# Optimization experiments

Hardware: AMD Instinct MI355X
Metric: run time of the kernel (lower is better)

Reference implementation:

```python
import jax, jax.numpy as jnp
import numpy as np

D_MODEL = 512
D_K = 64
D_V = 64
N_HEADS = 8
N = 4096
EPS = 1e-5


def setup_inputs() -> dict:
    key = jax.random.key(0)
    ks = jax.random.split(key, 12)
    s = 1.0 / np.sqrt(D_MODEL)
    return {
        "Q": jax.random.normal(ks[0], (N, D_MODEL), dtype=jnp.float32),
        "K": jax.random.normal(ks[1], (N, D_MODEL), dtype=jnp.float32),
        "V": jax.random.normal(ks[2], (N, D_MODEL), dtype=jnp.float32),
        "W_Q": jax.random.normal(ks[3], (D_K * N_HEADS, D_MODEL), dtype=jnp.float32) * s,
        "b_Q": jnp.zeros((D_K * N_HEADS,), jnp.float32),
        "W_K": jax.random.normal(ks[4], (D_K * N_HEADS, D_MODEL), dtype=jnp.float32) * s,
        "b_K": jnp.zeros((D_K * N_HEADS,), jnp.float32),
        "W_V": jax.random.normal(ks[5], (D_V * N_HEADS, D_MODEL), dtype=jnp.float32) * s,
        "b_V": jnp.zeros((D_V * N_HEADS,), jnp.float32),
        "W_O": jax.random.normal(ks[6], (D_MODEL, N_HEADS * D_V), dtype=jnp.float32) * s,
        "b_O": jnp.zeros((D_MODEL,), jnp.float32),
        "gamma": jnp.ones((D_MODEL,), jnp.float32),
        "beta": jnp.zeros((D_MODEL,), jnp.float32),
    }


def reference(Q, K, V, W_Q, b_Q, W_K, b_K, W_V, b_V, W_O, b_O, gamma, beta):
    n = Q.shape[0]
    # projections (torch Linear: x @ W.T + b), then split heads: [N, H, dk]
    Qs = (Q @ W_Q.T + b_Q).reshape(n, N_HEADS, D_K)
    Ks = (K @ W_K.T + b_K).reshape(n, N_HEADS, D_K)
    Vs = (V @ W_V.T + b_V).reshape(n, N_HEADS, D_V)
    # per-head scaled dot-product attention over the N dim, batched via einsum
    scores = jnp.einsum("nhd,mhd->hnm", Qs, Ks) / np.sqrt(D_K)  # [H, N, N]
    attn = jax.nn.softmax(scores, axis=-1)
    ctx = jnp.einsum("hnm,mhd->nhd", attn, Vs)  # [N, H, dv]
    context = ctx.reshape(n, N_HEADS * D_V)  # concat heads (matches torch.cat order)
    out = context @ W_O.T + b_O + Q  # output proj + residual
    # LayerNorm over last dim
    mu = jnp.mean(out, axis=-1, keepdims=True)
    var = jnp.mean((out - mu) ** 2, axis=-1, keepdims=True)
    return (out - mu) * jax.lax.rsqrt(var + EPS) * gamma + beta
```

## Files before the change

### kernel.cpp

```cpp
#include <hip/hip_runtime.h>
#include <cstdint>

#define N_TOK 4096
#define DMODEL 512
#define NHEADS 8
#define HDIM 64

typedef unsigned short u16;
typedef __bf16 bf16x8 __attribute__((ext_vector_type(8)));
typedef float f32x4 __attribute__((ext_vector_type(4)));

union U128 { uint4 u; bf16x8 b; u16 s[8]; };

__device__ __forceinline__ u16 f2bf(float f) {
  uint32_t u = __builtin_bit_cast(uint32_t, f);
  u += 0x7FFFu + ((u >> 16) & 1u);
  return (u16)(u >> 16);
}
__device__ __forceinline__ u16 bfr(float f) {
  uint32_t u = __builtin_bit_cast(uint32_t, f);
  return (u16)((u + 0x8000u) >> 16);
}
__device__ __forceinline__ float bf2f(u16 s) {
  uint32_t u = ((uint32_t)s) << 16;
  return __builtin_bit_cast(float, u);
}

#if __has_builtin(__builtin_amdgcn_exp2f)
#define EXP2(x) __builtin_amdgcn_exp2f(x)
#else
#define EXP2(x) __expf((x) * 0.6931471805599453f)
#endif

__device__ __forceinline__ void ldg2lds16(const void* g, void* s) {
  __builtin_amdgcn_global_load_lds(
      (const __attribute__((address_space(1))) void*)g,
      (__attribute__((address_space(3))) void*)s, 16, 0, 0);
}

__global__ __launch_bounds__(256) void cvt3_kernel(
    const float* __restrict__ a0, const float* __restrict__ a1, const float* __restrict__ a2,
    u16* __restrict__ b0, u16* __restrict__ b1, u16* __restrict__ b2)
{
  const float* src = (blockIdx.y == 0) ? a0 : (blockIdx.y == 1) ? a1 : a2;
  u16* dst         = (blockIdx.y == 0) ? b0 : (blockIdx.y == 1) ? b1 : b2;
  int i = (blockIdx.x * 256 + threadIdx.x) * 4;
  float4 f = *(const float4*)(src + i);
  ushort4 o;
  o.x = f2bf(f.x); o.y = f2bf(f.y); o.z = f2bf(f.z); o.w = f2bf(f.w);
  *(ushort4*)(dst + i) = o;
}

__global__ __launch_bounds__(256) void proj3_kernel(
    const u16* __restrict__ Qb, const u16* __restrict__ Kb, const u16* __restrict__ Vb,
    const float* __restrict__ WQ, const float* __restrict__ WK, const float* __restrict__ WV,
    const float* __restrict__ bQ, const float* __restrict__ bK, const float* __restrict__ bV,
    u16* __restrict__ Qs, u16* __restrict__ Ks, u16* __restrict__ Vt)
{
  const int z = blockIdx.z;
  const u16* A      = (z == 0) ? Qb : (z == 1) ? Kb : Vb;
  const float* W    = (z == 0) ? WQ : (z == 1) ? WK : WV;
  const float* bias = (z == 0) ? bQ : (z == 1) ? bK : bV;

  const int m0 = blockIdx.x * 128;
  const int j0 = blockIdx.y * 64;
  const int tid = threadIdx.x;
  const int w = tid >> 6, lane = tid & 63, quad = lane >> 4, l = lane & 15;

  __shared__ bf16x8 sA[8][128];
  __shared__ bf16x8 sB[8][64];

  const f32x4 zero = {0.f, 0.f, 0.f, 0.f};
  f32x4 acc[2][4];
#pragma unroll
  for (int m = 0; m < 2; ++m)
#pragma unroll
    for (int s = 0; s < 4; ++s) acc[m][s] = zero;

  const int brow0 = tid >> 3;
  const int bc    = tid & 7;

  for (int k0 = 0; k0 < DMODEL; k0 += 64) {
    __syncthreads();
#pragma unroll
    for (int i = 0; i < 4; ++i) {
      const int chunk = 2 * w + (i >> 1), half = (i & 1) * 64;
      const u16* ag = A + (size_t)(m0 + half + lane) * DMODEL + k0 + chunk * 8;
      ldg2lds16(ag, (char*)sA + (size_t)(chunk * 128 + half) * 16);
    }
#pragma unroll
    for (int i = 0; i < 2; ++i) {
      const int row = brow0 + 32 * i;
      const float* wp = W + (size_t)(j0 + row) * DMODEL + k0 + bc * 8;
      float4 g0 = *(const float4*)wp;
      float4 g1 = *(const float4*)(wp + 4);
      U128 v;
      v.s[0]=f2bf(g0.x); v.s[1]=f2bf(g0.y); v.s[2]=f2bf(g0.z); v.s[3]=f2bf(g0.w);
      v.s[4]=f2bf(g1.x); v.s[5]=f2bf(g1.y); v.s[6]=f2bf(g1.z); v.s[7]=f2bf(g1.w);
      sB[bc][row] = v.b;
    }
    __syncthreads();
#pragma unroll
    for (int c = 0; c < 2; ++c) {
      bf16x8 af0 = sA[c * 4 + quad][w * 32 + l];
      bf16x8 af1 = sA[c * 4 + quad][w * 32 + 16 + l];
#pragma unroll
      for (int s = 0; s < 4; ++s) {
        bf16x8 bfb = sB[c * 4 + quad][s * 16 + l];
        acc[0][s] = __builtin_amdgcn_mfma_f32_16x16x32_bf16(af0, bfb, acc[0][s], 0, 0, 0);
        acc[1][s] = __builtin_amdgcn_mfma_f32_16x16x32_bf16(af1, bfb, acc[1][s], 0, 0, 0);
      }
    }
  }

#pragma unroll
  for (int m = 0; m < 2; ++m)
#pragma unroll
    for (int s = 0; s < 4; ++s) {
      int j = j0 + s * 16 + l;
      float bv = bias[j];
      int n0 = m0 + w * 32 + m * 16 + quad * 4;
      if (z < 2) {
        u16* Y = (z == 0) ? Qs : Ks;
#pragma unroll
        for (int r = 0; r < 4; ++r)
          Y[(size_t)(n0 + r) * DMODEL + j] = f2bf(acc[m][s][r] + bv);
      } else {
        ushort4 pk;
        pk.x = f2bf(acc[m][s][0] + bv); pk.y = f2bf(acc[m][s][1] + bv);
        pk.z = f2bf(acc[m][s][2] + bv); pk.w = f2bf(acc[m][s][3] + bv);
        *(ushort4*)(Vt + (size_t)j * N_TOK + n0) = pk;
      }
    }
}

__global__ __launch_bounds__(512, 4) void attn_kernel(
    const u16* __restrict__ Qs, const u16* __restrict__ Ks,
    const u16* __restrict__ Vt, float* __restrict__ Opart, float* __restrict__ Lpart)
{
  const int qt = blockIdx.x, h = blockIdx.y, split = blockIdx.z;
  const int tid = threadIdx.x;
  const int w = tid >> 6, lane = tid & 63, quad = lane >> 4, l = lane & 15;

  __shared__ bf16x8 kch[8][64];
  __shared__ bf16x8 vch[8][64];
  __shared__ __align__(16) u16 pbuf[8][32][72];

  const int wq0 = qt * 256 + w * 32;

  bf16x8 qf[2][2];
#pragma unroll
  for (int c = 0; c < 2; ++c)
#pragma unroll
    for (int m = 0; m < 2; ++m) {
      U128 u;
      u.u = *(const uint4*)(Qs + (size_t)(wq0 + m * 16 + l) * DMODEL + h * HDIM + c * 32 + quad * 8);
#pragma unroll
      for (int j = 0; j < 8; ++j) u.s[j] = f2bf(bf2f(u.s[j]) * 0.18033688f);
      qf[c][m] = u.b;
    }

  const f32x4 zero = {0.f, 0.f, 0.f, 0.f};
  f32x4 o[2][4];
  float lsum[2] = {0.f, 0.f};
#pragma unroll
  for (int m = 0; m < 2; ++m)
#pragma unroll
    for (int s = 0; s < 4; ++s) o[m][s] = zero;

  for (int it = 0; it < 16; ++it) {
    const int j0 = split * 1024 + it * 64;
    __syncthreads();
    if (w < 4) {
      const u16* kg = Ks + (size_t)(j0 + lane) * DMODEL + h * HDIM + w * 16;
      ldg2lds16(kg,     (char*)kch + w * 2048);
      ldg2lds16(kg + 8, (char*)kch + w * 2048 + 1024);
    } else {
      const int w2 = w - 4;
      const u16* vg = Vt + (size_t)(h * HDIM + lane) * N_TOK + j0 + w2 * 16;
      ldg2lds16(vg,     (char*)vch + w2 * 2048);
      ldg2lds16(vg + 8, (char*)vch + w2 * 2048 + 1024);
    }
    __syncthreads();

    f32x4 sacc[2][4];
#pragma unroll
    for (int m = 0; m < 2; ++m)
#pragma unroll
      for (int t = 0; t < 4; ++t) sacc[m][t] = zero;
#pragma unroll
    for (int c = 0; c < 2; ++c) {
#pragma unroll
      for (int t = 0; t < 4; ++t) {
        bf16x8 kf = kch[c * 4 + quad][t * 16 + l];
        sacc[0][t] = __builtin_amdgcn_mfma_f32_16x16x32_bf16(kf, qf[c][0], sacc[0][t], 0, 0, 0);
        sacc[1][t] = __builtin_amdgcn_mfma_f32_16x16x32_bf16(kf, qf[c][1], sacc[1][t], 0, 0, 0);
      }
    }

#pragma unroll
    for (int m = 0; m < 2; ++m) {
#pragma unroll
      for (int t = 0; t < 4; ++t) {
        float p0 = EXP2(sacc[m][t][0]);
        float p1 = EXP2(sacc[m][t][1]);
        float p2 = EXP2(sacc[m][t][2]);
        float p3 = EXP2(sacc[m][t][3]);
        lsum[m] += (p0 + p1) + (p2 + p3);
        ushort4 pk;
        pk.x = bfr(p0); pk.y = bfr(p1); pk.z = bfr(p2); pk.w = bfr(p3);
        *(ushort4*)&pbuf[w][m * 16 + l][t * 16 + quad * 4] = pk;
      }
    }

#pragma unroll
    for (int c = 0; c < 2; ++c) {
      U128 u0, u1;
      u0.u = *(const uint4*)&pbuf[w][l][c * 32 + quad * 8];
      u1.u = *(const uint4*)&pbuf[w][16 + l][c * 32 + quad * 8];
#pragma unroll
      for (int s = 0; s < 4; ++s) {
        bf16x8 vf = vch[c * 4 + quad][s * 16 + l];
        o[0][s] = __builtin_amdgcn_mfma_f32_16x16x32_bf16(u0.b, vf, o[0][s], 0, 0, 0);
        o[1][s] = __builtin_amdgcn_mfma_f32_16x16x32_bf16(u1.b, vf, o[1][s], 0, 0, 0);
      }
    }
  }

#pragma unroll
  for (int m = 0; m < 2; ++m) {
    lsum[m] += __shfl_xor(lsum[m], 16);
    lsum[m] += __shfl_xor(lsum[m], 32);
  }
  if (quad == 0) {
    Lpart[((size_t)split * NHEADS + h) * N_TOK + wq0 + l]      = lsum[0];
    Lpart[((size_t)split * NHEADS + h) * N_TOK + wq0 + 16 + l] = lsum[1];
  }
  float* Ob = Opart + (size_t)((split * NHEADS + h) * 16 + qt) * 16384;
#pragma unroll
  for (int m = 0; m < 2; ++m)
#pragma unroll
    for (int s = 0; s < 4; ++s)
#pragma unroll
      for (int r = 0; r < 4; ++r)
        Ob[(w * 32 + m * 16 + quad * 4 + r) * 64 + s * 16 + l] = o[m][s][r];
}

__global__ __launch_bounds__(256) void combine_kernel(
    const float* __restrict__ Opart, const float* __restrict__ Lpart,
    u16* __restrict__ ctx)
{
  int idx = blockIdx.x * 256 + threadIdx.x;
  int n = idx >> 6;
  int c8 = idx & 63;
  int h = c8 >> 3;
  int vd0 = (c8 & 7) * 8;
  int qt = n >> 8, qin = n & 255;

  float acc[8] = {0, 0, 0, 0, 0, 0, 0, 0};
  float lsum = 0.f;
#pragma unroll
  for (int s = 0; s < 4; ++s) {
    size_t base = (size_t)((s * NHEADS + h) * 16 + qt) * 16384 + qin * 64 + vd0;
    float4 a = *(const float4*)(Opart + base);
    float4 b = *(const float4*)(Opart + base + 4);
    acc[0] += a.x; acc[1] += a.y; acc[2] += a.z; acc[3] += a.w;
    acc[4] += b.x; acc[5] += b.y; acc[6] += b.z; acc[7] += b.w;
    lsum += Lpart[((size_t)s * NHEADS + h) * N_TOK + n];
  }
  float inv = 1.f / lsum;
  U128 u;
#pragma unroll
  for (int j = 0; j < 8; ++j) u.s[j] = f2bf(acc[j] * inv);
  *(uint4*)(ctx + (size_t)n * DMODEL + h * HDIM + vd0) = u.u;
}

__global__ __launch_bounds__(256) void gemmo_kernel(
    const u16* __restrict__ ctx, const float* __restrict__ WO,
    const float* __restrict__ bO, const float* __restrict__ resid,
    float* __restrict__ Y)
{
  const int m0 = blockIdx.x * 64;
  const int j0 = blockIdx.y * 64;
  const int tid = threadIdx.x;
  const int w = tid >> 6, lane = tid & 63, quad = lane >> 4, l = lane & 15;

  __shared__ bf16x8 sA[8][64];
  __shared__ bf16x8 sB[8][64];

  const f32x4 zero = {0.f, 0.f, 0.f, 0.f};
  f32x4 acc[4];
  for (int s = 0; s < 4; ++s) acc[s] = zero;

  const int brow0 = tid >> 3;
  const int bc    = tid & 7;

  for (int k0 = 0; k0 < DMODEL; k0 += 64) {
    __syncthreads();
#pragma unroll
    for (int i = 0; i < 2; ++i) {
      const u16* ag = ctx + (size_t)(m0 + lane) * DMODEL + k0 + (2 * w + i) * 8;
      ldg2lds16(ag, (char*)sA + (size_t)(2 * w + i) * 1024);
    }
#pragma unroll
    for (int i = 0; i < 2; ++i) {
      const int row = brow0 + 32 * i;
      const float* wp = WO + (size_t)(j0 + row) * DMODEL + k0 + bc * 8;
      float4 g0 = *(const float4*)wp;
      float4 g1 = *(const float4*)(wp + 4);
      U128 v;
      v.s[0]=f2bf(g0.x); v.s[1]=f2bf(g0.y); v.s[2]=f2bf(g0.z); v.s[3]=f2bf(g0.w);
      v.s[4]=f2bf(g1.x); v.s[5]=f2bf(g1.y); v.s[6]=f2bf(g1.z); v.s[7]=f2bf(g1.w);
      sB[bc][row] = v.b;
    }
    __syncthreads();
#pragma unroll
    for (int c = 0; c < 2; ++c) {
      bf16x8 af = sA[c * 4 + quad][w * 16 + l];
#pragma unroll
      for (int s = 0; s < 4; ++s) {
        bf16x8 bfb = sB[c * 4 + quad][s * 16 + l];
        acc[s] = __builtin_amdgcn_mfma_f32_16x16x32_bf16(af, bfb, acc[s], 0, 0, 0);
      }
    }
  }
#pragma unroll
  for (int s = 0; s < 4; ++s) {
    int j = j0 + s * 16 + l;
    float bv = bO[j];
#pragma unroll
    for (int r = 0; r < 4; ++r) {
      int n = m0 + w * 16 + quad * 4 + r;
      Y[(size_t)n * DMODEL + j] = acc[s][r] + bv + resid[(size_t)n * DMODEL + j];
    }
  }
}

__global__ __launch_bounds__(256) void ln_kernel(
    const float* __restrict__ X, const float* __restrict__ gamma,
    const float* __restrict__ beta, float* __restrict__ Y)
{
  const int w = threadIdx.x >> 6, lane = threadIdx.x & 63;
  const int row = blockIdx.x * 4 + w;
  const float* x = X + (size_t)row * DMODEL + lane * 8;
  float4 a = *(const float4*)x;
  float4 b = *(const float4*)(x + 4);

  float s = a.x + a.y + a.z + a.w + b.x + b.y + b.z + b.w;
#pragma unroll
  for (int m = 1; m < 64; m <<= 1) s += __shfl_xor(s, m);
  float mu = s * (1.f / DMODEL);

  float d0 = a.x - mu, d1 = a.y - mu, d2 = a.z - mu, d3 = a.w - mu;
  float d4 = b.x - mu, d5 = b.y - mu, d6 = b.z - mu, d7 = b.w - mu;
  float v = d0*d0 + d1*d1 + d2*d2 + d3*d3 + d4*d4 + d5*d5 + d6*d6 + d7*d7;
#pragma unroll
  for (int m = 1; m < 64; m <<= 1) v += __shfl_xor(v, m);
  float sc = rsqrtf(v * (1.f / DMODEL) + 1e-5f);

  const float* g = gamma + lane * 8;
  const float* be = beta + lane * 8;
  float4 go = *(const float4*)g;
  float4 g1 = *(const float4*)(g + 4);
  float4 bo = *(const float4*)be;
  float4 b1 = *(const float4*)(be + 4);

  float4 y0, y1;
  y0.x = d0 * sc * go.x + bo.x;  y0.y = d1 * sc * go.y + bo.y;
  y0.z = d2 * sc * go.z + bo.z;  y0.w = d3 * sc * go.w + bo.w;
  y1.x = d4 * sc * g1.x + b1.x;  y1.y = d5 * sc * g1.y + b1.y;
  y1.z = d6 * sc * g1.z + b1.z;  y1.w = d7 * sc * g1.w + b1.w;

  float* yp = Y + (size_t)row * DMODEL + lane * 8;
  *(float4*)yp = y0;
  *(float4*)(yp + 4) = y1;
}

extern "C" void kernel_launch(void* const* d_in, const int* in_sizes, int n_in,
                              void* d_out, int out_size, void* d_ws, size_t ws_size,
                              hipStream_t stream)
{
  const float* Q     = (const float*)d_in[0];
  const float* K     = (const float*)d_in[1];
  const float* V     = (const float*)d_in[2];
  const float* WQ    = (const float*)d_in[3];
  const float* bQ    = (const float*)d_in[4];
  const float* WK    = (const float*)d_in[5];
  const float* bK    = (const float*)d_in[6];
  const float* WV    = (const float*)d_in[7];
  const float* bV    = (const float*)d_in[8];
  const float* WO    = (const float*)d_in[9];
  const float* bO    = (const float*)d_in[10];
  const float* gamma = (const float*)d_in[11];
  const float* beta  = (const float*)d_in[12];

  const size_t MB = 1ull << 20;
  char* ws = (char*)d_ws;
  u16* Qb   = (u16*)(ws + 0 * MB);
  u16* Kb   = (u16*)(ws + 4 * MB);
  u16* Vb   = (u16*)(ws + 8 * MB);
  u16* Qs   = (u16*)(ws + 12 * MB);
  u16* Ks   = (u16*)(ws + 16 * MB);
  u16* Vt   = (u16*)(ws + 20 * MB);
  u16* ctx  = (u16*)(ws + 24 * MB);
  float* Opart = (float*)(ws + 28 * MB);
  float* tmp   = (float*)(ws + 28 * MB);
  float* Lpart = (float*)(ws + 60 * MB);
  float* out = (float*)d_out;

  cvt3_kernel<<<dim3(2048, 3), 256, 0, stream>>>(Q, K, V, Qb, Kb, Vb);
  proj3_kernel<<<dim3(32, 8, 3), 256, 0, stream>>>(Qb, Kb, Vb, WQ, WK, WV,
                                                   bQ, bK, bV, Qs, Ks, Vt);
  attn_kernel<<<dim3(16, 8, 4), 512, 0, stream>>>(Qs, Ks, Vt, Opart, Lpart);
  combine_kernel<<<1024, 256, 0, stream>>>(Opart, Lpart, ctx);
  gemmo_kernel<<<dim3(64, 8), 256, 0, stream>>>(ctx, WO, bO, Q, tmp);
  ln_kernel<<<1024, 256, 0, stream>>>(tmp, gamma, beta, out);
}
```

Measured before the change: 187.5 us.

## Fuse input conversion into projection, widen attention tiles, store bf16 partials

Removes the separate fp32-to-bf16 conversion kernel and converts Q/K/V inside the projection GEMM while loading them into a padded LDS tile. The attention kernel moves to 256 threads with 64 query rows per wave, interleaves score and exp per key subtile, truncates P to bf16, and writes split partial outputs as bf16 in a contiguous layout. The combine kernel reads these bf16 partials, and the output GEMM uses 128-row tiles. This cuts launches and memory traffic at the cost of more register pressure in attention and lower precision in the partials.

```diff
diff --git a/kernel.cpp b/kernel.cpp
--- a/kernel.cpp
+++ b/kernel.cpp
@@ -17,14 +17,12 @@
   u += 0x7FFFu + ((u >> 16) & 1u);
   return (u16)(u >> 16);
 }
-__device__ __forceinline__ u16 bfr(float f) {
-  uint32_t u = __builtin_bit_cast(uint32_t, f);
-  return (u16)((u + 0x8000u) >> 16);
-}
 __device__ __forceinline__ float bf2f(u16 s) {
   uint32_t u = ((uint32_t)s) << 16;
   return __builtin_bit_cast(float, u);
 }
+__device__ __forceinline__ float bitf(uint32_t u) { return __builtin_bit_cast(float, u); }
+__device__ __forceinline__ uint32_t fbit(float f) { return __builtin_bit_cast(uint32_t, f); }
 
 #if __has_builtin(__builtin_amdgcn_exp2f)
 #define EXP2(x) __builtin_amdgcn_exp2f(x)
@@ -38,27 +36,14 @@
       (__attribute__((address_space(3))) void*)s, 16, 0, 0);
 }
 
-__global__ __launch_bounds__(256) void cvt3_kernel(
-    const float* __restrict__ a0, const float* __restrict__ a1, const float* __restrict__ a2,
-    u16* __restrict__ b0, u16* __restrict__ b1, u16* __restrict__ b2)
-{
-  const float* src = (blockIdx.y == 0) ? a0 : (blockIdx.y == 1) ? a1 : a2;
-  u16* dst         = (blockIdx.y == 0) ? b0 : (blockIdx.y == 1) ? b1 : b2;
-  int i = (blockIdx.x * 256 + threadIdx.x) * 4;
-  float4 f = *(const float4*)(src + i);
-  ushort4 o;
-  o.x = f2bf(f.x); o.y = f2bf(f.y); o.z = f2bf(f.z); o.w = f2bf(f.w);
-  *(ushort4*)(dst + i) = o;
-}
-
 __global__ __launch_bounds__(256) void proj3_kernel(
-    const u16* __restrict__ Qb, const u16* __restrict__ Kb, const u16* __restrict__ Vb,
+    const float* __restrict__ Qin, const float* __restrict__ Kin, const float* __restrict__ Vin,
     const float* __restrict__ WQ, const float* __restrict__ WK, const float* __restrict__ WV,
     const float* __restrict__ bQ, const float* __restrict__ bK, const float* __restrict__ bV,
     u16* __restrict__ Qs, u16* __restrict__ Ks, u16* __restrict__ Vt)
 {
   const int z = blockIdx.z;
-  const u16* A      = (z == 0) ? Qb : (z == 1) ? Kb : Vb;
+  const float* A    = (z == 0) ? Qin : (z == 1) ? Kin : Vin;
   const float* W    = (z == 0) ? WQ : (z == 1) ? WK : WV;
   const float* bias = (z == 0) ? bQ : (z == 1) ? bK : bV;
 
@@ -67,7 +52,7 @@
   const int tid = threadIdx.x;
   const int w = tid >> 6, lane = tid & 63, quad = lane >> 4, l = lane & 15;
 
-  __shared__ bf16x8 sA[8][128];
+  __shared__ __align__(16) u16 sAu[8 * 129 * 8];
   __shared__ bf16x8 sB[8][64];
 
   const f32x4 zero = {0.f, 0.f, 0.f, 0.f};
@@ -83,10 +68,16 @@
   for (int k0 = 0; k0 < DMODEL; k0 += 64) {
     __syncthreads();
 #pragma unroll
-    for (int i = 0; i < 4; ++i) {
-      const int chunk = 2 * w + (i >> 1), half = (i & 1) * 64;
-      const u16* ag = A + (size_t)(m0 + half + lane) * DMODEL + k0 + chunk * 8;
-      ldg2lds16(ag, (char*)sA + (size_t)(chunk * 128 + half) * 16);
+    for (int i = 0; i < 8; ++i) {
+      int flat4 = i * 256 + tid;
+      int f = flat4 * 4;
+      int row = f >> 6;
+      int col = f & 63;
+      float4 fv = *(const float4*)(A + (size_t)(m0 + row) * DMODEL + k0 + col);
+      ushort4 hh;
+      hh.x = f2bf(fv.x); hh.y = f2bf(fv.y); hh.z = f2bf(fv.z); hh.w = f2bf(fv.w);
+      int chunk = col >> 3, half = (col >> 2) & 1;
+      *(ushort4*)(sAu + ((chunk * 129 + row) << 3) + half * 4) = hh;
     }
 #pragma unroll
     for (int i = 0; i < 2; ++i) {
@@ -102,8 +93,8 @@
     __syncthreads();
 #pragma unroll
     for (int c = 0; c < 2; ++c) {
-      bf16x8 af0 = sA[c * 4 + quad][w * 32 + l];
-      bf16x8 af1 = sA[c * 4 + quad][w * 32 + 16 + l];
+      bf16x8 af0 = *(const bf16x8*)(sAu + (((c * 4 + quad) * 129 + w * 32 + l) << 3));
+      bf16x8 af1 = *(const bf16x8*)(sAu + (((c * 4 + quad) * 129 + w * 32 + 16 + l) << 3));
 #pragma unroll
       for (int s = 0; s < 4; ++s) {
         bf16x8 bfb = sB[c * 4 + quad][s * 16 + l];
@@ -134,9 +125,9 @@
     }
 }
 
-__global__ __launch_bounds__(512, 4) void attn_kernel(
+__global__ __launch_bounds__(256, 2) void attn_kernel(
     const u16* __restrict__ Qs, const u16* __restrict__ Ks,
-    const u16* __restrict__ Vt, float* __restrict__ Opart, float* __restrict__ Lpart)
+    const u16* __restrict__ Vt, u16* __restrict__ Opart, float* __restrict__ Lpart)
 {
   const int qt = blockIdx.x, h = blockIdx.y, split = blockIdx.z;
   const int tid = threadIdx.x;
@@ -144,15 +135,15 @@
 
   __shared__ bf16x8 kch[8][64];
   __shared__ bf16x8 vch[8][64];
-  __shared__ __align__(16) u16 pbuf[8][32][72];
-
-  const int wq0 = qt * 256 + w * 32;
-
-  bf16x8 qf[2][2];
+  __shared__ __align__(16) u16 pbuf[4][64][88];
+
+  const int wq0 = qt * 256 + w * 64;
+
+  bf16x8 qf[2][4];
 #pragma unroll
   for (int c = 0; c < 2; ++c)
 #pragma unroll
-    for (int m = 0; m < 2; ++m) {
+    for (int m = 0; m < 4; ++m) {
       U128 u;
       u.u = *(const uint4*)(Qs + (size_t)(wq0 + m * 16 + l) * DMODEL + h * HDIM + c * 32 + quad * 8);
 #pragma unroll
@@ -161,93 +152,100 @@
     }
 
   const f32x4 zero = {0.f, 0.f, 0.f, 0.f};
-  f32x4 o[2][4];
-  float lsum[2] = {0.f, 0.f};
-#pragma unroll
-  for (int m = 0; m < 2; ++m)
+  f32x4 o[4][4];
+  float lsum[4] = {0.f, 0.f, 0.f, 0.f};
+#pragma unroll
+  for (int m = 0; m < 4; ++m)
 #pragma unroll
     for (int s = 0; s < 4; ++s) o[m][s] = zero;
 
   for (int it = 0; it < 16; ++it) {
     const int j0 = split * 1024 + it * 64;
     __syncthreads();
-    if (w < 4) {
-      const u16* kg = Ks + (size_t)(j0 + lane) * DMODEL + h * HDIM + w * 16;
-      ldg2lds16(kg,     (char*)kch + w * 2048);
-      ldg2lds16(kg + 8, (char*)kch + w * 2048 + 1024);
+    if (w < 2) {
+#pragma unroll
+      for (int i = 0; i < 4; ++i) {
+        const int chunk = w * 4 + i;
+        const u16* kg = Ks + (size_t)(j0 + lane) * DMODEL + h * HDIM + chunk * 8;
+        ldg2lds16(kg, (char*)kch + chunk * 1024);
+      }
     } else {
-      const int w2 = w - 4;
-      const u16* vg = Vt + (size_t)(h * HDIM + lane) * N_TOK + j0 + w2 * 16;
-      ldg2lds16(vg,     (char*)vch + w2 * 2048);
-      ldg2lds16(vg + 8, (char*)vch + w2 * 2048 + 1024);
-    }
-    __syncthreads();
-
-    f32x4 sacc[2][4];
-#pragma unroll
-    for (int m = 0; m < 2; ++m)
-#pragma unroll
-      for (int t = 0; t < 4; ++t) sacc[m][t] = zero;
+#pragma unroll
+      for (int i = 0; i < 4; ++i) {
+        const int chunk = (w - 2) * 4 + i;
+        const u16* vg = Vt + (size_t)(h * HDIM + lane) * N_TOK + j0 + chunk * 8;
+        ldg2lds16(vg, (char*)vch + chunk * 1024);
+      }
+    }
+    __syncthreads();
+
+#pragma unroll
+    for (int t = 0; t < 4; ++t) {
+      f32x4 sacc[4];
+#pragma unroll
+      for (int m = 0; m < 4; ++m) sacc[m] = zero;
+#pragma unroll
+      for (int c = 0; c < 2; ++c) {
+        bf16x8 kf = kch[c * 4 + quad][t * 16 + l];
+        sacc[0] = __builtin_amdgcn_mfma_f32_16x16x32_bf16(kf, qf[c][0], sacc[0], 0, 0, 0);
+        sacc[1] = __builtin_amdgcn_mfma_f32_16x16x32_bf16(kf, qf[c][1], sacc[1], 0, 0, 0);
+        sacc[2] = __builtin_amdgcn_mfma_f32_16x16x32_bf16(kf, qf[c][2], sacc[2], 0, 0, 0);
+        sacc[3] = __builtin_amdgcn_mfma_f32_16x16x32_bf16(kf, qf[c][3], sacc[3], 0, 0, 0);
+      }
+#pragma unroll
+      for (int m = 0; m < 4; ++m) {
+        uint32_t u0 = fbit(EXP2(sacc[m][0]));
+        uint32_t u1 = fbit(EXP2(sacc[m][1]));
+        uint32_t u2 = fbit(EXP2(sacc[m][2]));
+        uint32_t u3 = fbit(EXP2(sacc[m][3]));
+        uint32_t pk01 = (u0 >> 16) | (u1 & 0xFFFF0000u);
+        uint32_t pk23 = (u2 >> 16) | (u3 & 0xFFFF0000u);
+        lsum[m] += (bitf(pk01 << 16) + bitf(pk01 & 0xFFFF0000u)) +
+                   (bitf(pk23 << 16) + bitf(pk23 & 0xFFFF0000u));
+        uint2 st; st.x = pk01; st.y = pk23;
+        *(uint2*)&pbuf[w][m * 16 + l][t * 16 + quad * 4] = st;
+      }
+    }
+
 #pragma unroll
     for (int c = 0; c < 2; ++c) {
-#pragma unroll
-      for (int t = 0; t < 4; ++t) {
-        bf16x8 kf = kch[c * 4 + quad][t * 16 + l];
-        sacc[0][t] = __builtin_amdgcn_mfma_f32_16x16x32_bf16(kf, qf[c][0], sacc[0][t], 0, 0, 0);
-        sacc[1][t] = __builtin_amdgcn_mfma_f32_16x16x32_bf16(kf, qf[c][1], sacc[1][t], 0, 0, 0);
-      }
-    }
-
-#pragma unroll
-    for (int m = 0; m < 2; ++m) {
-#pragma unroll
-      for (int t = 0; t < 4; ++t) {
-        float p0 = EXP2(sacc[m][t][0]);
-        float p1 = EXP2(sacc[m][t][1]);
-        float p2 = EXP2(sacc[m][t][2]);
-        float p3 = EXP2(sacc[m][t][3]);
-        lsum[m] += (p0 + p1) + (p2 + p3);
-        ushort4 pk;
-        pk.x = bfr(p0); pk.y = bfr(p1); pk.z = bfr(p2); pk.w = bfr(p3);
-        *(ushort4*)&pbuf[w][m * 16 + l][t * 16 + quad * 4] = pk;
-      }
-    }
-
-#pragma unroll
-    for (int c = 0; c < 2; ++c) {
-      U128 u0, u1;
-      u0.u = *(const uint4*)&pbuf[w][l][c * 32 + quad * 8];
-      u1.u = *(const uint4*)&pbuf[w][16 + l][c * 32 + quad * 8];
+      U128 pf[4];
+#pragma unroll
+      for (int m = 0; m < 4; ++m)
+        pf[m].u = *(const uint4*)&pbuf[w][m * 16 + l][c * 32 + quad * 8];
 #pragma unroll
       for (int s = 0; s < 4; ++s) {
         bf16x8 vf = vch[c * 4 + quad][s * 16 + l];
-        o[0][s] = __builtin_amdgcn_mfma_f32_16x16x32_bf16(u0.b, vf, o[0][s], 0, 0, 0);
-        o[1][s] = __builtin_amdgcn_mfma_f32_16x16x32_bf16(u1.b, vf, o[1][s], 0, 0, 0);
-      }
-    }
-  }
-
-#pragma unroll
-  for (int m = 0; m < 2; ++m) {
+        o[0][s] = __builtin_amdgcn_mfma_f32_16x16x32_bf16(pf[0].b, vf, o[0][s], 0, 0, 0);
+        o[1][s] = __builtin_amdgcn_mfma_f32_16x16x32_bf16(pf[1].b, vf, o[1][s], 0, 0, 0);
+        o[2][s] = __builtin_amdgcn_mfma_f32_16x16x32_bf16(pf[2].b, vf, o[2][s], 0, 0, 0);
+        o[3][s] = __builtin_amdgcn_mfma_f32_16x16x32_bf16(pf[3].b, vf, o[3][s], 0, 0, 0);
+      }
+    }
+  }
+
+#pragma unroll
+  for (int m = 0; m < 4; ++m) {
     lsum[m] += __shfl_xor(lsum[m], 16);
     lsum[m] += __shfl_xor(lsum[m], 32);
   }
   if (quad == 0) {
-    Lpart[((size_t)split * NHEADS + h) * N_TOK + wq0 + l]      = lsum[0];
-    Lpart[((size_t)split * NHEADS + h) * N_TOK + wq0 + 16 + l] = lsum[1];
-  }
-  float* Ob = Opart + (size_t)((split * NHEADS + h) * 16 + qt) * 16384;
-#pragma unroll
-  for (int m = 0; m < 2; ++m)
+#pragma unroll
+    for (int m = 0; m < 4; ++m)
+      Lpart[((size_t)split * NHEADS + h) * N_TOK + wq0 + m * 16 + l] = lsum[m];
+  }
+  u16* Ob = Opart + ((size_t)(split * NHEADS + h) * N_TOK + wq0) * 64;
+#pragma unroll
+  for (int m = 0; m < 4; ++m)
 #pragma unroll
     for (int s = 0; s < 4; ++s)
 #pragma unroll
       for (int r = 0; r < 4; ++r)
-        Ob[(w * 32 + m * 16 + quad * 4 + r) * 64 + s * 16 + l] = o[m][s][r];
+        Ob[(size_t)(m * 16 + quad * 4 + r) * 64 + s * 16 + l] = f2bf(o[m][s][r]);
 }
 
 __global__ __launch_bounds__(256) void combine_kernel(
-    const float* __restrict__ Opart, const float* __restrict__ Lpart,
+    const u16* __restrict__ Opart, const float* __restrict__ Lpart,
     u16* __restrict__ ctx)
 {
   int idx = blockIdx.x * 256 + threadIdx.x;
@@ -255,17 +253,15 @@
   int c8 = idx & 63;
   int h = c8 >> 3;
   int vd0 = (c8 & 7) * 8;
-  int qt = n >> 8, qin = n & 255;
 
   float acc[8] = {0, 0, 0, 0, 0, 0, 0, 0};
   float lsum = 0.f;
 #pragma unroll
   for (int s = 0; s < 4; ++s) {
-    size_t base = (size_t)((s * NHEADS + h) * 16 + qt) * 16384 + qin * 64 + vd0;
-    float4 a = *(const float4*)(Opart + base);
-    float4 b = *(const float4*)(Opart + base + 4);
-    acc[0] += a.x; acc[1] += a.y; acc[2] += a.z; acc[3] += a.w;
-    acc[4] += b.x; acc[5] += b.y; acc[6] += b.z; acc[7] += b.w;
+    U128 u;
+    u.u = *(const uint4*)(Opart + ((size_t)(s * NHEADS + h) * N_TOK + n) * 64 + vd0);
+#pragma unroll
+    for (int j = 0; j < 8; ++j) acc[j] += bf2f(u.s[j]);
     lsum += Lpart[((size_t)s * NHEADS + h) * N_TOK + n];
   }
   float inv = 1.f / lsum;
@@ -280,17 +276,20 @@
     const float* __restrict__ bO, const float* __restrict__ resid,
     float* __restrict__ Y)
 {
-  const int m0 = blockIdx.x * 64;
+  const int m0 = blockIdx.x * 128;
   const int j0 = blockIdx.y * 64;
   const int tid = threadIdx.x;
   const int w = tid >> 6, lane = tid & 63, quad = lane >> 4, l = lane & 15;
 
-  __shared__ bf16x8 sA[8][64];
+  __shared__ bf16x8 sA[8][128];
   __shared__ bf16x8 sB[8][64];
 
   const f32x4 zero = {0.f, 0.f, 0.f, 0.f};
-  f32x4 acc[4];
-  for (int s = 0; s < 4; ++s) acc[s] = zero;
+  f32x4 acc[2][4];
+#pragma unroll
+  for (int m = 0; m < 2; ++m)
+#pragma unroll
+    for (int s = 0; s < 4; ++s) acc[m][s] = zero;
 
   const int brow0 = tid >> 3;
   const int bc    = tid & 7;
@@ -298,9 +297,10 @@
   for (int k0 = 0; k0 < DMODEL; k0 += 64) {
     __syncthreads();
 #pragma unroll
-    for (int i = 0; i < 2; ++i) {
-      const u16* ag = ctx + (size_t)(m0 + lane) * DMODEL + k0 + (2 * w + i) * 8;
-      ldg2lds16(ag, (char*)sA + (size_t)(2 * w + i) * 1024);
+    for (int i = 0; i < 4; ++i) {
+      const int chunk = 2 * w + (i >> 1), half = (i & 1) * 64;
+      const u16* ag = ctx + (size_t)(m0 + half + lane) * DMODEL + k0 + chunk * 8;
+      ldg2lds16(ag, (char*)sA + (size_t)(chunk * 128 + half) * 16);
     }
 #pragma unroll
     for (int i = 0; i < 2; ++i) {
@@ -316,24 +316,27 @@
     __syncthreads();
 #pragma unroll
     for (int c = 0; c < 2; ++c) {
-      bf16x8 af = sA[c * 4 + quad][w * 16 + l];
+      bf16x8 af0 = sA[c * 4 + quad][w * 32 + l];
+      bf16x8 af1 = sA[c * 4 + quad][w * 32 + 16 + l];
 #pragma unroll
       for (int s = 0; s < 4; ++s) {
         bf16x8 bfb = sB[c * 4 + quad][s * 16 + l];
-        acc[s] = __builtin_amdgcn_mfma_f32_16x16x32_bf16(af, bfb, acc[s], 0, 0, 0);
-      }
-    }
-  }
-#pragma unroll
-  for (int s = 0; s < 4; ++s) {
-    int j = j0 + s * 16 + l;
-    float bv = bO[j];
-#pragma unroll
-    for (int r = 0; r < 4; ++r) {
-      int n = m0 + w * 16 + quad * 4 + r;
-      Y[(size_t)n * DMODEL + j] = acc[s][r] + bv + resid[(size_t)n * DMODEL + j];
-    }
-  }
+        acc[0][s] = __builtin_amdgcn_mfma_f32_16x16x32_bf16(af0, bfb, acc[0][s], 0, 0, 0);
+        acc[1][s] = __builtin_amdgcn_mfma_f32_16x16x32_bf16(af1, bfb, acc[1][s], 0, 0, 0);
+      }
+    }
+  }
+#pragma unroll
+  for (int m = 0; m < 2; ++m)
+#pragma unroll
+    for (int s = 0; s < 4; ++s) {
+      int j = j0 + s * 16 + l;
+      float bv = bO[j];
+      int n0 = m0 + w * 32 + m * 16 + quad * 4;
+#pragma unroll
+      for (int r = 0; r < 4; ++r)
+        Y[(size_t)(n0 + r) * DMODEL + j] = acc[m][s][r] + bv + resid[(size_t)(n0 + r) * DMODEL + j];
+    }
 }
 
 __global__ __launch_bounds__(256) void ln_kernel(
@@ -396,23 +399,19 @@
 
   const size_t MB = 1ull << 20;
   char* ws = (char*)d_ws;
-  u16* Qb   = (u16*)(ws + 0 * MB);
-  u16* Kb   = (u16*)(ws + 4 * MB);
-  u16* Vb   = (u16*)(ws + 8 * MB);
-  u16* Qs   = (u16*)(ws + 12 * MB);
-  u16* Ks   = (u16*)(ws + 16 * MB);
-  u16* Vt   = (u16*)(ws + 20 * MB);
-  u16* ctx  = (u16*)(ws + 24 * MB);
-  float* Opart = (float*)(ws + 28 * MB);
-  float* tmp   = (float*)(ws + 28 * MB);
-  float* Lpart = (float*)(ws + 60 * MB);
+  u16* Qs   = (u16*)(ws + 0 * MB);
+  u16* Ks   = (u16*)(ws + 4 * MB);
+  u16* Vt   = (u16*)(ws + 8 * MB);
+  u16* ctx  = (u16*)(ws + 12 * MB);
+  u16* Opart = (u16*)(ws + 16 * MB);
+  float* tmp = (float*)(ws + 16 * MB);
+  float* Lpart = (float*)(ws + 32 * MB);
   float* out = (float*)d_out;
 
-  cvt3_kernel<<<dim3(2048, 3), 256, 0, stream>>>(Q, K, V, Qb, Kb, Vb);
-  proj3_kernel<<<dim3(32, 8, 3), 256, 0, stream>>>(Qb, Kb, Vb, WQ, WK, WV,
+  proj3_kernel<<<dim3(32, 8, 3), 256, 0, stream>>>(Q, K, V, WQ, WK, WV,
                                                    bQ, bK, bV, Qs, Ks, Vt);
-  attn_kernel<<<dim3(16, 8, 4), 512, 0, stream>>>(Qs, Ks, Vt, Opart, Lpart);
+  attn_kernel<<<dim3(16, 8, 4), 256, 0, stream>>>(Qs, Ks, Vt, Opart, Lpart);
   combine_kernel<<<1024, 256, 0, stream>>>(Opart, Lpart, ctx);
-  gemmo_kernel<<<dim3(64, 8), 256, 0, stream>>>(ctx, WO, bO, Q, tmp);
+  gemmo_kernel<<<dim3(32, 8), 256, 0, stream>>>(ctx, WO, bO, Q, tmp);
   ln_kernel<<<1024, 256, 0, stream>>>(tmp, gamma, beta, out);
 }
```

Result: slower. 196.6 us (+4.9%).

## Pre-convert weights to bf16, double-buffer GEMM/attention tiles, store partial outputs as bf16

Applied to the files above, without the earlier changes.

Weights are now converted to bf16 once in a merged conversion kernel, so both projection GEMMs load bf16 tiles straight into LDS with async loads instead of converting fp32 in the inner loop. The projection, output-projection and attention loops get double-buffered LDS staging, so the next tile's loads overlap current compute and one barrier per iteration is dropped. Attention partial outputs are written as bf16 instead of fp32 and the grid is reordered, and the output GEMM tile grows to 128 rows. The costs are extra LDS use, lost precision in the partial sums, and softmax probabilities now truncated rather than rounded to bf16.

```diff
diff --git a/kernel.cpp b/kernel.cpp
--- a/kernel.cpp
+++ b/kernel.cpp
@@ -17,14 +17,11 @@
   u += 0x7FFFu + ((u >> 16) & 1u);
   return (u16)(u >> 16);
 }
-__device__ __forceinline__ u16 bfr(float f) {
-  uint32_t u = __builtin_bit_cast(uint32_t, f);
-  return (u16)((u + 0x8000u) >> 16);
-}
 __device__ __forceinline__ float bf2f(u16 s) {
   uint32_t u = ((uint32_t)s) << 16;
   return __builtin_bit_cast(float, u);
 }
+__device__ __forceinline__ uint32_t fbit(float f) { return __builtin_bit_cast(uint32_t, f); }
 
 #if __has_builtin(__builtin_amdgcn_exp2f)
 #define EXP2(x) __builtin_amdgcn_exp2f(x)
@@ -38,13 +35,24 @@
       (__attribute__((address_space(3))) void*)s, 16, 0, 0);
 }
 
-__global__ __launch_bounds__(256) void cvt3_kernel(
-    const float* __restrict__ a0, const float* __restrict__ a1, const float* __restrict__ a2,
-    u16* __restrict__ b0, u16* __restrict__ b1, u16* __restrict__ b2)
-{
-  const float* src = (blockIdx.y == 0) ? a0 : (blockIdx.y == 1) ? a1 : a2;
-  u16* dst         = (blockIdx.y == 0) ? b0 : (blockIdx.y == 1) ? b1 : b2;
-  int i = (blockIdx.x * 256 + threadIdx.x) * 4;
+__global__ __launch_bounds__(256) void cvt7_kernel(
+    const float* __restrict__ Q, const float* __restrict__ K, const float* __restrict__ V,
+    const float* __restrict__ WQ, const float* __restrict__ WK, const float* __restrict__ WV,
+    const float* __restrict__ WO,
+    u16* __restrict__ Qb, u16* __restrict__ Kb, u16* __restrict__ Vb,
+    u16* __restrict__ WQb, u16* __restrict__ WKb, u16* __restrict__ WVb,
+    u16* __restrict__ WOb)
+{
+  int b = blockIdx.x;
+  const float* src; u16* dst; int rel;
+  if      (b < 2048) { src = Q;  dst = Qb;  rel = b; }
+  else if (b < 4096) { src = K;  dst = Kb;  rel = b - 2048; }
+  else if (b < 6144) { src = V;  dst = Vb;  rel = b - 4096; }
+  else if (b < 6400) { src = WQ; dst = WQb; rel = b - 6144; }
+  else if (b < 6656) { src = WK; dst = WKb; rel = b - 6400; }
+  else if (b < 6912) { src = WV; dst = WVb; rel = b - 6656; }
+  else               { src = WO; dst = WOb; rel = b - 6912; }
+  int i = (rel * 256 + threadIdx.x) * 4;
   float4 f = *(const float4*)(src + i);
   ushort4 o;
   o.x = f2bf(f.x); o.y = f2bf(f.y); o.z = f2bf(f.z); o.w = f2bf(f.w);
@@ -53,13 +61,13 @@
 
 __global__ __launch_bounds__(256) void proj3_kernel(
     const u16* __restrict__ Qb, const u16* __restrict__ Kb, const u16* __restrict__ Vb,
-    const float* __restrict__ WQ, const float* __restrict__ WK, const float* __restrict__ WV,
+    const u16* __restrict__ WQb, const u16* __restrict__ WKb, const u16* __restrict__ WVb,
     const float* __restrict__ bQ, const float* __restrict__ bK, const float* __restrict__ bV,
     u16* __restrict__ Qs, u16* __restrict__ Ks, u16* __restrict__ Vt)
 {
   const int z = blockIdx.z;
   const u16* A      = (z == 0) ? Qb : (z == 1) ? Kb : Vb;
-  const float* W    = (z == 0) ? WQ : (z == 1) ? WK : WV;
+  const u16* W      = (z == 0) ? WQb : (z == 1) ? WKb : WVb;
   const float* bias = (z == 0) ? bQ : (z == 1) ? bK : bV;
 
   const int m0 = blockIdx.x * 128;
@@ -67,8 +75,8 @@
   const int tid = threadIdx.x;
   const int w = tid >> 6, lane = tid & 63, quad = lane >> 4, l = lane & 15;
 
-  __shared__ bf16x8 sA[8][128];
-  __shared__ bf16x8 sB[8][64];
+  __shared__ bf16x8 sA[2][8][128];
+  __shared__ bf16x8 sB[2][8][64];
 
   const f32x4 zero = {0.f, 0.f, 0.f, 0.f};
   f32x4 acc[2][4];
@@ -77,40 +85,39 @@
 #pragma unroll
     for (int s = 0; s < 4; ++s) acc[m][s] = zero;
 
-  const int brow0 = tid >> 3;
-  const int bc    = tid & 7;
-
-  for (int k0 = 0; k0 < DMODEL; k0 += 64) {
-    __syncthreads();
+  auto stage = [&](int kt, int buf) {
+    const int k0 = kt * 64;
 #pragma unroll
     for (int i = 0; i < 4; ++i) {
       const int chunk = 2 * w + (i >> 1), half = (i & 1) * 64;
       const u16* ag = A + (size_t)(m0 + half + lane) * DMODEL + k0 + chunk * 8;
-      ldg2lds16(ag, (char*)sA + (size_t)(chunk * 128 + half) * 16);
+      ldg2lds16(ag, (char*)&sA[buf][chunk][half]);
     }
 #pragma unroll
     for (int i = 0; i < 2; ++i) {
-      const int row = brow0 + 32 * i;
-      const float* wp = W + (size_t)(j0 + row) * DMODEL + k0 + bc * 8;
-      float4 g0 = *(const float4*)wp;
-      float4 g1 = *(const float4*)(wp + 4);
-      U128 v;
-      v.s[0]=f2bf(g0.x); v.s[1]=f2bf(g0.y); v.s[2]=f2bf(g0.z); v.s[3]=f2bf(g0.w);
-      v.s[4]=f2bf(g1.x); v.s[5]=f2bf(g1.y); v.s[6]=f2bf(g1.z); v.s[7]=f2bf(g1.w);
-      sB[bc][row] = v.b;
-    }
-    __syncthreads();
+      const int chunk = 2 * w + i;
+      const u16* bg = W + (size_t)(j0 + lane) * DMODEL + k0 + chunk * 8;
+      ldg2lds16(bg, (char*)&sB[buf][chunk][0]);
+    }
+  };
+
+  stage(0, 0);
+  __syncthreads();
+  for (int kt = 0; kt < 8; ++kt) {
+    const int buf = kt & 1;
+    if (kt + 1 < 8) stage(kt + 1, buf ^ 1);
 #pragma unroll
     for (int c = 0; c < 2; ++c) {
-      bf16x8 af0 = sA[c * 4 + quad][w * 32 + l];
-      bf16x8 af1 = sA[c * 4 + quad][w * 32 + 16 + l];
+      bf16x8 af0 = sA[buf][c * 4 + quad][w * 32 + l];
+      bf16x8 af1 = sA[buf][c * 4 + quad][w * 32 + 16 + l];
 #pragma unroll
       for (int s = 0; s < 4; ++s) {
-        bf16x8 bfb = sB[c * 4 + quad][s * 16 + l];
+        bf16x8 bfb = sB[buf][c * 4 + quad][s * 16 + l];
         acc[0][s] = __builtin_amdgcn_mfma_f32_16x16x32_bf16(af0, bfb, acc[0][s], 0, 0, 0);
         acc[1][s] = __builtin_amdgcn_mfma_f32_16x16x32_bf16(af1, bfb, acc[1][s], 0, 0, 0);
       }
     }
+    __syncthreads();
   }
 
 #pragma unroll
@@ -136,14 +143,16 @@
 
 __global__ __launch_bounds__(512, 4) void attn_kernel(
     const u16* __restrict__ Qs, const u16* __restrict__ Ks,
-    const u16* __restrict__ Vt, float* __restrict__ Opart, float* __restrict__ Lpart)
-{
-  const int qt = blockIdx.x, h = blockIdx.y, split = blockIdx.z;
+    const u16* __restrict__ Vt, u16* __restrict__ Opart, float* __restrict__ Lpart)
+{
+  const int hs = blockIdx.x;
+  const int h = hs & 7, split = hs >> 3;
+  const int qt = blockIdx.y;
   const int tid = threadIdx.x;
   const int w = tid >> 6, lane = tid & 63, quad = lane >> 4, l = lane & 15;
 
-  __shared__ bf16x8 kch[8][64];
-  __shared__ bf16x8 vch[8][64];
+  __shared__ bf16x8 kch[2][8][64];
+  __shared__ bf16x8 vch[2][8][64];
   __shared__ __align__(16) u16 pbuf[8][32][72];
 
   const int wq0 = qt * 256 + w * 32;
@@ -168,63 +177,64 @@
 #pragma unroll
     for (int s = 0; s < 4; ++s) o[m][s] = zero;
 
-  for (int it = 0; it < 16; ++it) {
+  auto stage = [&](int it, int buf) {
     const int j0 = split * 1024 + it * 64;
-    __syncthreads();
     if (w < 4) {
       const u16* kg = Ks + (size_t)(j0 + lane) * DMODEL + h * HDIM + w * 16;
-      ldg2lds16(kg,     (char*)kch + w * 2048);
-      ldg2lds16(kg + 8, (char*)kch + w * 2048 + 1024);
+      ldg2lds16(kg,     (char*)&kch[buf][2 * w][0]);
+      ldg2lds16(kg + 8, (char*)&kch[buf][2 * w + 1][0]);
     } else {
       const int w2 = w - 4;
       const u16* vg = Vt + (size_t)(h * HDIM + lane) * N_TOK + j0 + w2 * 16;
-      ldg2lds16(vg,     (char*)vch + w2 * 2048);
-      ldg2lds16(vg + 8, (char*)vch + w2 * 2048 + 1024);
+      ldg2lds16(vg,     (char*)&vch[buf][2 * w2][0]);
+      ldg2lds16(vg + 8, (char*)&vch[buf][2 * w2 + 1][0]);
+    }
+  };
+
+  stage(0, 0);
+  __syncthreads();
+
+  for (int it = 0; it < 16; ++it) {
+    const int buf = it & 1;
+    if (it + 1 < 16) stage(it + 1, buf ^ 1);
+
+#pragma unroll
+    for (int t = 0; t < 4; ++t) {
+      f32x4 sacc[2];
+      sacc[0] = zero; sacc[1] = zero;
+#pragma unroll
+      for (int c = 0; c < 2; ++c) {
+        bf16x8 kf = kch[buf][c * 4 + quad][t * 16 + l];
+        sacc[0] = __builtin_amdgcn_mfma_f32_16x16x32_bf16(kf, qf[c][0], sacc[0], 0, 0, 0);
+        sacc[1] = __builtin_amdgcn_mfma_f32_16x16x32_bf16(kf, qf[c][1], sacc[1], 0, 0, 0);
+      }
+#pragma unroll
+      for (int m = 0; m < 2; ++m) {
+        float p0 = EXP2(sacc[m][0]);
+        float p1 = EXP2(sacc[m][1]);
+        float p2 = EXP2(sacc[m][2]);
+        float p3 = EXP2(sacc[m][3]);
+        lsum[m] += (p0 + p1) + (p2 + p3);
+        uint32_t pk01 = (fbit(p0) >> 16) | (fbit(p1) & 0xFFFF0000u);
+        uint32_t pk23 = (fbit(p2) >> 16) | (fbit(p3) & 0xFFFF0000u);
+        uint2 st; st.x = pk01; st.y = pk23;
+        *(uint2*)&pbuf[w][m * 16 + l][t * 16 + quad * 4] = st;
+      }
+    }
+
+#pragma unroll
+    for (int c = 0; c < 2; ++c) {
+      U128 pf0, pf1;
+      pf0.u = *(const uint4*)&pbuf[w][l][c * 32 + quad * 8];
+      pf1.u = *(const uint4*)&pbuf[w][16 + l][c * 32 + quad * 8];
+#pragma unroll
+      for (int s = 0; s < 4; ++s) {
+        bf16x8 vf = vch[buf][c * 4 + quad][s * 16 + l];
+        o[0][s] = __builtin_amdgcn_mfma_f32_16x16x32_bf16(pf0.b, vf, o[0][s], 0, 0, 0);
+        o[1][s] = __builtin_amdgcn_mfma_f32_16x16x32_bf16(pf1.b, vf, o[1][s], 0, 0, 0);
+      }
     }
     __syncthreads();
-
-    f32x4 sacc[2][4];
-#pragma unroll
-    for (int m = 0; m < 2; ++m)
-#pragma unroll
-      for (int t = 0; t < 4; ++t) sacc[m][t] = zero;
-#pragma unroll
-    for (int c = 0; c < 2; ++c) {
-#pragma unroll
-      for (int t = 0; t < 4; ++t) {
-        bf16x8 kf = kch[c * 4 + quad][t * 16 + l];
-        sacc[0][t] = __builtin_amdgcn_mfma_f32_16x16x32_bf16(kf, qf[c][0], sacc[0][t], 0, 0, 0);
-        sacc[1][t] = __builtin_amdgcn_mfma_f32_16x16x32_bf16(kf, qf[c][1], sacc[1][t], 0, 0, 0);
-      }
-    }
-
-#pragma unroll
-    for (int m = 0; m < 2; ++m) {
-#pragma unroll
-      for (int t = 0; t < 4; ++t) {
-        float p0 = EXP2(sacc[m][t][0]);
-        float p1 = EXP2(sacc[m][t][1]);
-        float p2 = EXP2(sacc[m][t][2]);
-        float p3 = EXP2(sacc[m][t][3]);
-        lsum[m] += (p0 + p1) + (p2 + p3);
-        ushort4 pk;
-        pk.x = bfr(p0); pk.y = bfr(p1); pk.z = bfr(p2); pk.w = bfr(p3);
-        *(ushort4*)&pbuf[w][m * 16 + l][t * 16 + quad * 4] = pk;
-      }
-    }
-
-#pragma unroll
-    for (int c = 0; c < 2; ++c) {
-      U128 u0, u1;
-      u0.u = *(const uint4*)&pbuf[w][l][c * 32 + quad * 8];
-      u1.u = *(const uint4*)&pbuf[w][16 + l][c * 32 + quad * 8];
-#pragma unroll
-      for (int s = 0; s < 4; ++s) {
-        bf16x8 vf = vch[c * 4 + quad][s * 16 + l];
-        o[0][s] = __builtin_amdgcn_mfma_f32_16x16x32_bf16(u0.b, vf, o[0][s], 0, 0, 0);
-        o[1][s] = __builtin_amdgcn_mfma_f32_16x16x32_bf16(u1.b, vf, o[1][s], 0, 0, 0);
-      }
-    }
   }
 
 #pragma unroll
@@ -236,18 +246,18 @@
     Lpart[((size_t)split * NHEADS + h) * N_TOK + wq0 + l]      = lsum[0];
     Lpart[((size_t)split * NHEADS + h) * N_TOK + wq0 + 16 + l] = lsum[1];
   }
-  float* Ob = Opart + (size_t)((split * NHEADS + h) * 16 + qt) * 16384;
+  u16* Ob = Opart + ((size_t)(split * NHEADS + h) * N_TOK + wq0) * 64;
 #pragma unroll
   for (int m = 0; m < 2; ++m)
 #pragma unroll
     for (int s = 0; s < 4; ++s)
 #pragma unroll
       for (int r = 0; r < 4; ++r)
-        Ob[(w * 32 + m * 16 + quad * 4 + r) * 64 + s * 16 + l] = o[m][s][r];
+        Ob[(size_t)(m * 16 + quad * 4 + r) * 64 + s * 16 + l] = f2bf(o[m][s][r]);
 }
 
 __global__ __launch_bounds__(256) void combine_kernel(
-    const float* __restrict__ Opart, const float* __restrict__ Lpart,
+    const u16* __restrict__ Opart, const float* __restrict__ Lpart,
     u16* __restrict__ ctx)
 {
   int idx = blockIdx.x * 256 + threadIdx.x;
@@ -255,17 +265,15 @@
   int c8 = idx & 63;
   int h = c8 >> 3;
   int vd0 = (c8 & 7) * 8;
-  int qt = n >> 8, qin = n & 255;
 
   float acc[8] = {0, 0, 0, 0, 0, 0, 0, 0};
   float lsum = 0.f;
 #pragma unroll
   for (int s = 0; s < 4; ++s) {
-    size_t base = (size_t)((s * NHEADS + h) * 16 + qt) * 16384 + qin * 64 + vd0;
-    float4 a = *(const float4*)(Opart + base);
-    float4 b = *(const float4*)(Opart + base + 4);
-    acc[0] += a.x; acc[1] += a.y; acc[2] += a.z; acc[3] += a.w;
-    acc[4] += b.x; acc[5] += b.y; acc[6] += b.z; acc[7] += b.w;
+    U128 u;
+    u.u = *(const uint4*)(Opart + ((size_t)(s * NHEADS + h) * N_TOK + n) * 64 + vd0);
+#pragma unroll
+    for (int j = 0; j < 8; ++j) acc[j] += bf2f(u.s[j]);
     lsum += Lpart[((size_t)s * NHEADS + h) * N_TOK + n];
   }
   float inv = 1.f / lsum;
@@ -276,64 +284,70 @@
 }
 
 __global__ __launch_bounds__(256) void gemmo_kernel(
-    const u16* __restrict__ ctx, const float* __restrict__ WO,
+    const u16* __restrict__ ctx, const u16* __restrict__ WOb,
     const float* __restrict__ bO, const float* __restrict__ resid,
     float* __restrict__ Y)
 {
-  const int m0 = blockIdx.x * 64;
+  const int m0 = blockIdx.x * 128;
   const int j0 = blockIdx.y * 64;
   const int tid = threadIdx.x;
   const int w = tid >> 6, lane = tid & 63, quad = lane >> 4, l = lane & 15;
 
-  __shared__ bf16x8 sA[8][64];
-  __shared__ bf16x8 sB[8][64];
+  __shared__ bf16x8 sA[2][8][128];
+  __shared__ bf16x8 sB[2][8][64];
 
   const f32x4 zero = {0.f, 0.f, 0.f, 0.f};
-  f32x4 acc[4];
-  for (int s = 0; s < 4; ++s) acc[s] = zero;
-
-  const int brow0 = tid >> 3;
-  const int bc    = tid & 7;
-
-  for (int k0 = 0; k0 < DMODEL; k0 += 64) {
+  f32x4 acc[2][4];
+#pragma unroll
+  for (int m = 0; m < 2; ++m)
+#pragma unroll
+    for (int s = 0; s < 4; ++s) acc[m][s] = zero;
+
+  auto stage = [&](int kt, int buf) {
+    const int k0 = kt * 64;
+#pragma unroll
+    for (int i = 0; i < 4; ++i) {
+      const int chunk = 2 * w + (i >> 1), half = (i & 1) * 64;
+      const u16* ag = ctx + (size_t)(m0 + half + lane) * DMODEL + k0 + chunk * 8;
+      ldg2lds16(ag, (char*)&sA[buf][chunk][half]);
+    }
+#pragma unroll
+    for (int i = 0; i < 2; ++i) {
+      const int chunk = 2 * w + i;
+      const u16* bg = WOb + (size_t)(j0 + lane) * DMODEL + k0 + chunk * 8;
+      ldg2lds16(bg, (char*)&sB[buf][chunk][0]);
+    }
+  };
+
+  stage(0, 0);
+  __syncthreads();
+  for (int kt = 0; kt < 8; ++kt) {
+    const int buf = kt & 1;
+    if (kt + 1 < 8) stage(kt + 1, buf ^ 1);
+#pragma unroll
+    for (int c = 0; c < 2; ++c) {
+      bf16x8 af0 = sA[buf][c * 4 + quad][w * 32 + l];
+      bf16x8 af1 = sA[buf][c * 4 + quad][w * 32 + 16 + l];
+#pragma unroll
+      for (int s = 0; s < 4; ++s) {
+        bf16x8 bfb = sB[buf][c * 4 + quad][s * 16 + l];
+        acc[0][s] = __builtin_amdgcn_mfma_f32_16x16x32_bf16(af0, bfb, acc[0][s], 0, 0, 0);
+        acc[1][s] = __builtin_amdgcn_mfma_f32_16x16x32_bf16(af1, bfb, acc[1][s], 0, 0, 0);
+      }
+    }
     __syncthreads();
-#pragma unroll
-    for (int i = 0; i < 2; ++i) {
-      const u16* ag = ctx + (size_t)(m0 + lane) * DMODEL + k0 + (2 * w + i) * 8;
-      ldg2lds16(ag, (char*)sA + (size_t)(2 * w + i) * 1024);
-    }
-#pragma unroll
-    for (int i = 0; i < 2; ++i) {
-      const int row = brow0 + 32 * i;
-      const float* wp = WO + (size_t)(j0 + row) * DMODEL + k0 + bc * 8;
-      float4 g0 = *(const float4*)wp;
-      float4 g1 = *(const float4*)(wp + 4);
-      U128 v;
-      v.s[0]=f2bf(g0.x); v.s[1]=f2bf(g0.y); v.s[2]=f2bf(g0.z); v.s[3]=f2bf(g0.w);
-      v.s[4]=f2bf(g1.x); v.s[5]=f2bf(g1.y); v.s[6]=f2bf(g1.z); v.s[7]=f2bf(g1.w);
-      sB[bc][row] = v.b;
-    }
-    __syncthreads();
-#pragma unroll
-    for (int c = 0; c < 2; ++c) {
-      bf16x8 af = sA[c * 4 + quad][w * 16 + l];
-#pragma unroll
-      for (int s = 0; s < 4; ++s) {
-        bf16x8 bfb = sB[c * 4 + quad][s * 16 + l];
-        acc[s] = __builtin_amdgcn_mfma_f32_16x16x32_bf16(af, bfb, acc[s], 0, 0, 0);
-      }
-    }
-  }
-#pragma unroll
-  for (int s = 0; s < 4; ++s) {
-    int j = j0 + s * 16 + l;
-    float bv = bO[j];
-#pragma unroll
-    for (int r = 0; r < 4; ++r) {
-      int n = m0 + w * 16 + quad * 4 + r;
-      Y[(size_t)n * DMODEL + j] = acc[s][r] + bv + resid[(size_t)n * DMODEL + j];
-    }
-  }
+  }
+#pragma unroll
+  for (int m = 0; m < 2; ++m)
+#pragma unroll
+    for (int s = 0; s < 4; ++s) {
+      int j = j0 + s * 16 + l;
+      float bv = bO[j];
+      int n0 = m0 + w * 32 + m * 16 + quad * 4;
+#pragma unroll
+      for (int r = 0; r < 4; ++r)
+        Y[(size_t)(n0 + r) * DMODEL + j] = acc[m][s][r] + bv + resid[(size_t)(n0 + r) * DMODEL + j];
+    }
 }
 
 __global__ __launch_bounds__(256) void ln_kernel(
@@ -399,20 +413,25 @@
   u16* Qb   = (u16*)(ws + 0 * MB);
   u16* Kb   = (u16*)(ws + 4 * MB);
   u16* Vb   = (u16*)(ws + 8 * MB);
-  u16* Qs   = (u16*)(ws + 12 * MB);
-  u16* Ks   = (u16*)(ws + 16 * MB);
-  u16* Vt   = (u16*)(ws + 20 * MB);
-  u16* ctx  = (u16*)(ws + 24 * MB);
-  float* Opart = (float*)(ws + 28 * MB);
-  float* tmp   = (float*)(ws + 28 * MB);
-  float* Lpart = (float*)(ws + 60 * MB);
+  u16* WQb  = (u16*)(ws + 12 * MB);
+  u16* WKb  = (u16*)(ws + 12 * MB + 512 * 1024);
+  u16* WVb  = (u16*)(ws + 13 * MB);
+  u16* WOb  = (u16*)(ws + 13 * MB + 512 * 1024);
+  u16* Qs   = (u16*)(ws + 14 * MB);
+  u16* Ks   = (u16*)(ws + 18 * MB);
+  u16* Vt   = (u16*)(ws + 22 * MB);
+  u16* ctx  = (u16*)(ws + 26 * MB);
+  u16* Opart = (u16*)(ws + 30 * MB);
+  float* tmp = (float*)(ws + 30 * MB);
+  float* Lpart = (float*)(ws + 46 * MB);
   float* out = (float*)d_out;
 
-  cvt3_kernel<<<dim3(2048, 3), 256, 0, stream>>>(Q, K, V, Qb, Kb, Vb);
-  proj3_kernel<<<dim3(32, 8, 3), 256, 0, stream>>>(Qb, Kb, Vb, WQ, WK, WV,
+  cvt7_kernel<<<7168, 256, 0, stream>>>(Q, K, V, WQ, WK, WV, WO,
+                                        Qb, Kb, Vb, WQb, WKb, WVb, WOb);
+  proj3_kernel<<<dim3(32, 8, 3), 256, 0, stream>>>(Qb, Kb, Vb, WQb, WKb, WVb,
                                                    bQ, bK, bV, Qs, Ks, Vt);
-  attn_kernel<<<dim3(16, 8, 4), 512, 0, stream>>>(Qs, Ks, Vt, Opart, Lpart);
+  attn_kernel<<<dim3(32, 16), 512, 0, stream>>>(Qs, Ks, Vt, Opart, Lpart);
   combine_kernel<<<1024, 256, 0, stream>>>(Opart, Lpart, ctx);
-  gemmo_kernel<<<dim3(64, 8), 256, 0, stream>>>(ctx, WO, bO, Q, tmp);
+  gemmo_kernel<<<dim3(32, 8), 256, 0, stream>>>(ctx, WOb, bO, Q, tmp);
   ln_kernel<<<1024, 256, 0, stream>>>(tmp, gamma, beta, out);
 }
```

After: 185.0 us. Within noise of the previous version (-1.4%).
